# Kernel tuning notes

Measured on AMD Instinct MI355X. Metric: run time of the kernel, lower is better.

The kernel has to match this reference:

```python
import jax, jax.numpy as jnp
import numpy as np

BERT_DIM = 1024
HIDDEN = 64          # GlobalPointer head size d
NUM_TYPE = 9
MASK_NEG = 1.0e12


def _rope_sin_cos(seq_len, dim, dtype=jnp.float32):
    # sinusoidal_position_embedding: emb[s, 2i]=sin(s*w_i), emb[s,2i+1]=cos(s*w_i)
    pos = jnp.arange(seq_len, dtype=dtype)[:, None]                  # [S,1]
    inv = jnp.power(10000.0, -2.0 * jnp.arange(dim // 2, dtype=dtype) / dim)
    ang = pos * inv                                                   # [S,D/2]
    sin_pos = jnp.repeat(jnp.sin(ang), 2, axis=-1)                    # [S,D] = emb[..., ::2] interleave-2
    cos_pos = jnp.repeat(jnp.cos(ang), 2, axis=-1)                    # [S,D] = emb[..., 1::2] interleave-2
    return sin_pos, cos_pos


def _rotate(x):
    # stack([-x[...,1::2], x[...,::2]], -1).reshape(x.shape)
    x2 = jnp.stack([-x[..., 1::2], x[..., ::2]], axis=-1)
    return x2.reshape(x.shape)


def setup_inputs() -> dict:
    key = jax.random.key(0)
    k1, k2, k3 = jax.random.split(key, 3)
    B, S = 16, 512
    hidden = jax.random.normal(k1, (B, S, BERT_DIM), dtype=jnp.float32)
    attention_mask = jnp.ones((B, S), dtype=jnp.float32)
    W = jax.random.normal(k2, (BERT_DIM, NUM_TYPE * HIDDEN * 2), dtype=jnp.float32) * (1.0 / np.sqrt(BERT_DIM))
    b = jax.random.normal(k3, (NUM_TYPE * HIDDEN * 2,), dtype=jnp.float32) * 0.02
    return {"bert_last_hidden_state": hidden, "attention_mask": attention_mask, "W": W, "b": b}


def reference(bert_last_hidden_state, attention_mask, W, b):
    h = bert_last_hidden_state                                        # [B,S,bert_dim]
    B, S, _ = h.shape
    out = h @ W + b                                                   # [B,S,T*2d]
    # split into T chunks of 2d and stack on dim -2 == reshape
    out = out.reshape(B, S, NUM_TYPE, 2 * HIDDEN)
    qw, kw = out[..., :HIDDEN], out[..., HIDDEN:]                     # [B,S,T,d]
    sin_pos, cos_pos = _rope_sin_cos(S, HIDDEN, h.dtype)              # [S,d]
    sin_pos = sin_pos[None, :, None, :]                               # [1,S,1,d]
    cos_pos = cos_pos[None, :, None, :]
    qw = qw * cos_pos + _rotate(qw) * sin_pos
    kw = kw * cos_pos + _rotate(kw) * sin_pos
    logits = jnp.einsum('bmhd,bnhd->bhmn', qw, kw)                    # [B,T,S,S]
    pad = attention_mask[:, None, None, :]                            # [B,1,1,S] -> broadcast [B,T,S,S]
    logits = logits * pad - (1.0 - pad) * MASK_NEG
    return logits / jnp.sqrt(jnp.asarray(HIDDEN, logits.dtype))
```

## Files before the change

kernel.cpp:

```cpp
#include <hip/hip_runtime.h>
#include <hip/hip_bf16.h>

#define BDIM 1024
#define NCOL 1152
#define HEADS 9
#define HID 64
#define SLEN 512
#define BATCH 16

typedef __attribute__((ext_vector_type(8))) short bf16x8;
typedef __attribute__((ext_vector_type(8))) unsigned short u16x8;
typedef __attribute__((ext_vector_type(4))) float f32x4;
typedef __attribute__((ext_vector_type(4))) unsigned short u16x4;

static __device__ __forceinline__ unsigned short f2bf(float f) {
    union { float f; unsigned int u; } x; x.f = f;
    unsigned int u = x.u;
    unsigned int r = (u + 0x7fffu + ((u >> 16) & 1u)) >> 16;
    return (unsigned short)r;
}

#define GLOAD_LDS16(g, l)                                                     \
    __builtin_amdgcn_global_load_lds(                                         \
        (const __attribute__((address_space(1))) unsigned int*)(g),           \
        (__attribute__((address_space(3))) unsigned int*)(l), 16, 0, 0)

__global__ __launch_bounds__(256) void prep_kernel(const float* __restrict__ hidden,
                                                   const float* __restrict__ W,
                                                   unsigned short* __restrict__ Ab,
                                                   unsigned short* __restrict__ Wt,
                                                   float* __restrict__ sctab) {
    __shared__ float tile[32][33];
    const int b = blockIdx.x;
    if (b < 4096) {
        int i = (b * 256 + threadIdx.x) * 8;
        float4 a = *reinterpret_cast<const float4*>(hidden + i);
        float4 c = *reinterpret_cast<const float4*>(hidden + i + 4);
        u16x8 p;
        p[0] = f2bf(a.x); p[1] = f2bf(a.y); p[2] = f2bf(a.z); p[3] = f2bf(a.w);
        p[4] = f2bf(c.x); p[5] = f2bf(c.y); p[6] = f2bf(c.z); p[7] = f2bf(c.w);
        *reinterpret_cast<u16x8*>(Ab + i) = p;
    } else if (b < 5248) {
        const int bb = b - 4096;
        const int tx = threadIdx.x & 31;
        const int ty = threadIdx.x >> 5;
        const int nb = (bb % 36) * 32;
        const int kb = (bb / 36) * 32;
#pragma unroll
        for (int i = 0; i < 4; ++i) {
            int k = kb + ty + i * 8;
            tile[ty + i * 8][tx] = W[(size_t)k * NCOL + nb + tx];
        }
        __syncthreads();
#pragma unroll
        for (int i = 0; i < 4; ++i) {
            int n = nb + ty + i * 8;
            Wt[(size_t)n * BDIM + kb + tx] = f2bf(tile[tx][ty + i * 8]);
        }
    } else {
        int idx = (b - 5248) * 256 + threadIdx.x;
        int s = idx >> 5, j = idx & 31;
        float inv = powf(10000.0f, -(float)(2 * j) / (float)HID);
        float ang = (float)s * inv;
        sctab[idx * 2]     = sinf(ang);
        sctab[idx * 2 + 1] = cosf(ang);
    }
}

__global__ __launch_bounds__(512) void proj_rope_kernel(
    const unsigned short* __restrict__ Ab,
    const unsigned short* __restrict__ Wt,
    const float* __restrict__ bias,
    const float4* __restrict__ sctab4,
    unsigned short* __restrict__ qk)
{
    __shared__ __attribute__((aligned(16))) unsigned short As[2][256 * 64];
    __shared__ __attribute__((aligned(16))) unsigned short Bs[2][192 * 64];

    const int t = threadIdx.x;
    const int m0 = blockIdx.x * 256;
    const int n0 = blockIdx.y * 144;
    const int wid = t >> 6, lane = t & 63;
    const int lrow = lane & 15;
    const int lk = lane >> 4;

    const int rowoff = lane >> 3;
    const int sslot = (lane & 7) ^ rowoff;
    const unsigned short* gA = Ab + (size_t)(m0 + wid * 32 + rowoff) * BDIM + sslot * 8;
    const unsigned short* gB = Wt + (size_t)(n0 + wid * 24 + rowoff) * BDIM + sslot * 8;
    const int lA = wid * 2048;
    const int lB = wid * 1536;

#define STAGE(buf, k0)                                                        \
    do {                                                                      \
        GLOAD_LDS16(gA + (k0),             &As[buf][lA]);                     \
        GLOAD_LDS16(gA + (k0) + 8 * BDIM,  &As[buf][lA + 512]);               \
        GLOAD_LDS16(gA + (k0) + 16 * BDIM, &As[buf][lA + 1024]);              \
        GLOAD_LDS16(gA + (k0) + 24 * BDIM, &As[buf][lA + 1536]);              \
        GLOAD_LDS16(gB + (k0),             &Bs[buf][lB]);                     \
        GLOAD_LDS16(gB + (k0) + 8 * BDIM,  &Bs[buf][lB + 512]);               \
        GLOAD_LDS16(gB + (k0) + 16 * BDIM, &Bs[buf][lB + 1024]);              \
    } while (0)

    const int rkey = lrow & 7;

    f32x4 acc[9][2] = {};

    STAGE(0, 0);
    asm volatile("s_waitcnt vmcnt(0)" ::: "memory");
    __builtin_amdgcn_s_barrier();
    __builtin_amdgcn_sched_barrier(0);

    int cur = 0;
    for (int it = 0; it < 16; ++it) {
        if (it < 15) STAGE(cur ^ 1, (it + 1) * 64);
        __builtin_amdgcn_sched_barrier(0);

        const char* Ac = (const char*)As[cur];
        const char* Bc = (const char*)Bs[cur];
#pragma unroll
        for (int kk = 0; kk < 2; ++kk) {
            const int fslot = ((kk * 4 + lk) ^ rkey) << 4;
            bf16x8 af[2], bfr[9];
#pragma unroll
            for (int mi = 0; mi < 2; ++mi)
                af[mi] = *reinterpret_cast<const bf16x8*>(
                    Ac + (wid * 32 + mi * 16 + lrow) * 128 + fslot);
#pragma unroll
            for (int ni = 0; ni < 9; ++ni)
                bfr[ni] = *reinterpret_cast<const bf16x8*>(
                    Bc + (ni * 16 + lrow) * 128 + fslot);
#pragma unroll
            for (int ni = 0; ni < 9; ++ni)
#pragma unroll
                for (int mi = 0; mi < 2; ++mi)
                    acc[ni][mi] = __builtin_amdgcn_mfma_f32_16x16x32_bf16(
                        bfr[ni], af[mi], acc[ni][mi], 0, 0, 0);
        }

        if (it < 15) {
            asm volatile("s_waitcnt vmcnt(0)" ::: "memory");
            __builtin_amdgcn_s_barrier();
            __builtin_amdgcn_sched_barrier(0);
        }
        cur ^= 1;
    }
#undef STAGE

    const float4* bias4 = (const float4*)bias;
#pragma unroll
    for (int ni = 0; ni < 9; ++ni) {
        int cb = n0 + ni * 16 + lk * 4;
        float4 bv = bias4[cb >> 2];
        int h = cb >> 7;
        int qki = (cb >> 6) & 1;
        int d0 = cb & 63;
#pragma unroll
        for (int mi = 0; mi < 2; ++mi) {
            int m = m0 + wid * 32 + mi * 16 + lrow;
            int bi = m >> 9, s = m & 511;
            float4 sc = sctab4[s * 16 + (d0 >> 2)];
            f32x4 a = acc[ni][mi];
            float v0 = a[0] + bv.x, v1 = a[1] + bv.y;
            float v2 = a[2] + bv.z, v3 = a[3] + bv.w;
            u16x4 p;
            p[0] = f2bf(v0 * sc.y - v1 * sc.x);
            p[1] = f2bf(v1 * sc.y + v0 * sc.x);
            p[2] = f2bf(v2 * sc.w - v3 * sc.z);
            p[3] = f2bf(v3 * sc.w + v2 * sc.z);
            *reinterpret_cast<u16x4*>(
                qk + ((((size_t)bi * HEADS + h) * 2 + qki) * SLEN + s) * HID + d0) = p;
        }
    }
}

__global__ __launch_bounds__(256) void logits_kernel(
    const unsigned short* __restrict__ qkbuf,
    const float* __restrict__ mask,
    float* __restrict__ out)
{
    __shared__ __attribute__((aligned(16))) unsigned short Qs[128 * 72];
    __shared__ __attribute__((aligned(16))) unsigned short Ks[128 * 72];

    const int t = threadIdx.x;
    const int bz = blockIdx.z;
    const int bi = bz / 9;
    const int m0 = blockIdx.x * 128, n0 = blockIdx.y * 128;

    const unsigned short* Qg = qkbuf + ((size_t)bz * 2 + 0) * SLEN * HID + (size_t)m0 * HID;
    const unsigned short* Kg = qkbuf + ((size_t)bz * 2 + 1) * SLEN * HID + (size_t)n0 * HID;

#pragma unroll
    for (int i = 0; i < 4; ++i) {
        int e = t + i * 256;
        int row = e >> 3, c = e & 7;
        *reinterpret_cast<uint4*>(&Qs[row * 72 + c * 8]) =
            *reinterpret_cast<const uint4*>(Qg + (size_t)row * HID + c * 8);
        *reinterpret_cast<uint4*>(&Ks[row * 72 + c * 8]) =
            *reinterpret_cast<const uint4*>(Kg + (size_t)row * HID + c * 8);
    }
    __syncthreads();

    const int wid = t >> 6, lane = t & 63;
    const int wr = wid >> 1, wc = wid & 1;
    const int lrow = lane & 15;
    const int lk = lane >> 4;

    f32x4 acc[4][4] = {};
#pragma unroll
    for (int kk = 0; kk < 2; ++kk) {
        bf16x8 af[4], bfr[4];
#pragma unroll
        for (int mi = 0; mi < 4; ++mi)
            af[mi] = *reinterpret_cast<const bf16x8*>(
                &Qs[(wr * 64 + mi * 16 + lrow) * 72 + kk * 32 + lk * 8]);
#pragma unroll
        for (int ni = 0; ni < 4; ++ni)
            bfr[ni] = *reinterpret_cast<const bf16x8*>(
                &Ks[(wc * 64 + ni * 16 + lrow) * 72 + kk * 32 + lk * 8]);
#pragma unroll
        for (int ni = 0; ni < 4; ++ni)
#pragma unroll
            for (int mi = 0; mi < 4; ++mi)
                acc[ni][mi] = __builtin_amdgcn_mfma_f32_16x16x32_bf16(
                    bfr[ni], af[mi], acc[ni][mi], 0, 0, 0);
    }

#pragma unroll
    for (int ni = 0; ni < 4; ++ni) {
        int nb = n0 + wc * 64 + ni * 16 + lk * 4;
        float4 pv = *reinterpret_cast<const float4*>(mask + bi * SLEN + nb);
        float sx = (1.0f - pv.x) * 1000000000000.0f;
        float sy = (1.0f - pv.y) * 1000000000000.0f;
        float sz = (1.0f - pv.z) * 1000000000000.0f;
        float sw = (1.0f - pv.w) * 1000000000000.0f;
#pragma unroll
        for (int mi = 0; mi < 4; ++mi) {
            int m = m0 + wr * 64 + mi * 16 + lrow;
            f32x4 a = acc[ni][mi];
            f32x4 o;
            o[0] = (a[0] * pv.x - sx) * 0.125f;
            o[1] = (a[1] * pv.y - sy) * 0.125f;
            o[2] = (a[2] * pv.z - sz) * 0.125f;
            o[3] = (a[3] * pv.w - sw) * 0.125f;
            *reinterpret_cast<f32x4*>(out + ((size_t)bz * SLEN + m) * SLEN + nb) = o;
        }
    }
}

extern "C" void kernel_launch(void* const* d_in, const int* in_sizes, int n_in,
                              void* d_out, int out_size, void* d_ws, size_t ws_size,
                              hipStream_t stream) {
    const float* hidden = (const float*)d_in[0];
    const float* mask   = (const float*)d_in[1];
    const float* W      = (const float*)d_in[2];
    const float* bias   = (const float*)d_in[3];
    float* out = (float*)d_out;

    char* ws = (char*)d_ws;
    unsigned short* Ab = (unsigned short*)ws;
    unsigned short* Wt = (unsigned short*)(ws + 16777216);
    float* sctab = (float*)(ws + 16777216 + 2457600);
    unsigned short* qk = (unsigned short*)(ws + 16777216 + 2457600 + 131072);

    prep_kernel<<<5312, 256, 0, stream>>>(hidden, W, Ab, Wt, sctab);
    proj_rope_kernel<<<dim3(32, 8), 512, 0, stream>>>(
        Ab, Wt, bias, (const float4*)sctab, qk);
    logits_kernel<<<dim3(4, 4, BATCH * HEADS), 256, 0, stream>>>(qk, mask, out);
}
```

Before: 84.95 us.

## Triple-buffer projection GEMM LDS with split-phase prefetch and MFMA priority

Changes the projection GEMM from double to triple-buffered LDS staging. Prefetch runs two k-tiles ahead, with the A and B loads split across the two k sub-phases and per-wave vmcnt waits. Only the first 6 waves load B, and the B buffer shrinks to the 144 rows actually used. It also raises wave priority around the MFMA bursts and shrinks the workspace layout for Wt. The aim is to hide global-load latency behind compute, at the cost of more LDS (less occupancy headroom) and tricky wait-count correctness.

```diff
diff --git a/kernel.cpp b/kernel.cpp
--- a/kernel.cpp
+++ b/kernel.cpp
@@ -74,8 +74,8 @@
     const float4* __restrict__ sctab4,
     unsigned short* __restrict__ qk)
 {
-    __shared__ __attribute__((aligned(16))) unsigned short As[2][256 * 64];
-    __shared__ __attribute__((aligned(16))) unsigned short Bs[2][192 * 64];
+    __shared__ __attribute__((aligned(16))) unsigned short As[3][256 * 64];
+    __shared__ __attribute__((aligned(16))) unsigned short Bs[3][144 * 64];
 
     const int t = threadIdx.x;
     const int m0 = blockIdx.x * 256;
@@ -90,13 +90,17 @@
     const unsigned short* gB = Wt + (size_t)(n0 + wid * 24 + rowoff) * BDIM + sslot * 8;
     const int lA = wid * 2048;
     const int lB = wid * 1536;
-
-#define STAGE(buf, k0)                                                        \
+    const bool hasB = (wid < 6);
+
+#define STAGE_A(buf, k0)                                                      \
     do {                                                                      \
         GLOAD_LDS16(gA + (k0),             &As[buf][lA]);                     \
         GLOAD_LDS16(gA + (k0) + 8 * BDIM,  &As[buf][lA + 512]);               \
         GLOAD_LDS16(gA + (k0) + 16 * BDIM, &As[buf][lA + 1024]);              \
         GLOAD_LDS16(gA + (k0) + 24 * BDIM, &As[buf][lA + 1536]);              \
+    } while (0)
+#define STAGE_B(buf, k0)                                                      \
+    do {                                                                      \
         GLOAD_LDS16(gB + (k0),             &Bs[buf][lB]);                     \
         GLOAD_LDS16(gB + (k0) + 8 * BDIM,  &Bs[buf][lB + 512]);               \
         GLOAD_LDS16(gB + (k0) + 16 * BDIM, &Bs[buf][lB + 1024]);              \
@@ -106,21 +110,26 @@
 
     f32x4 acc[9][2] = {};
 
-    STAGE(0, 0);
-    asm volatile("s_waitcnt vmcnt(0)" ::: "memory");
-    __builtin_amdgcn_s_barrier();
-    __builtin_amdgcn_sched_barrier(0);
+    STAGE_A(0, 0);  if (hasB) STAGE_B(0, 0);
+    STAGE_A(1, 64); if (hasB) STAGE_B(1, 64);
 
     int cur = 0;
     for (int it = 0; it < 16; ++it) {
-        if (it < 15) STAGE(cur ^ 1, (it + 1) * 64);
+        if (it < 15) {
+            if (hasB) asm volatile("s_waitcnt vmcnt(7)" ::: "memory");
+            else      asm volatile("s_waitcnt vmcnt(4)" ::: "memory");
+        } else {
+            asm volatile("s_waitcnt vmcnt(0)" ::: "memory");
+        }
+        __builtin_amdgcn_s_barrier();
         __builtin_amdgcn_sched_barrier(0);
 
         const char* Ac = (const char*)As[cur];
         const char* Bc = (const char*)Bs[cur];
-#pragma unroll
-        for (int kk = 0; kk < 2; ++kk) {
-            const int fslot = ((kk * 4 + lk) ^ rkey) << 4;
+        const int nb2 = (cur + 2 >= 3) ? cur - 1 : cur + 2;
+
+        {
+            const int fslot = (lk ^ rkey) << 4;
             bf16x8 af[2], bfr[9];
 #pragma unroll
             for (int mi = 0; mi < 2; ++mi)
@@ -130,22 +139,51 @@
             for (int ni = 0; ni < 9; ++ni)
                 bfr[ni] = *reinterpret_cast<const bf16x8*>(
                     Bc + (ni * 16 + lrow) * 128 + fslot);
+            if (it < 14) STAGE_A(nb2, (it + 2) * 64);
+            __builtin_amdgcn_sched_barrier(0);
+            asm volatile("s_waitcnt lgkmcnt(0)" ::: "memory");
+            __builtin_amdgcn_sched_barrier(0);
+            __builtin_amdgcn_s_setprio(1);
 #pragma unroll
             for (int ni = 0; ni < 9; ++ni)
 #pragma unroll
                 for (int mi = 0; mi < 2; ++mi)
                     acc[ni][mi] = __builtin_amdgcn_mfma_f32_16x16x32_bf16(
                         bfr[ni], af[mi], acc[ni][mi], 0, 0, 0);
-        }
-
-        if (it < 15) {
-            asm volatile("s_waitcnt vmcnt(0)" ::: "memory");
-            __builtin_amdgcn_s_barrier();
+            __builtin_amdgcn_s_setprio(0);
+        }
+        __builtin_amdgcn_s_barrier();
+        __builtin_amdgcn_sched_barrier(0);
+
+        {
+            const int fslot = ((4 + lk) ^ rkey) << 4;
+            bf16x8 af[2], bfr[9];
+#pragma unroll
+            for (int mi = 0; mi < 2; ++mi)
+                af[mi] = *reinterpret_cast<const bf16x8*>(
+                    Ac + (wid * 32 + mi * 16 + lrow) * 128 + fslot);
+#pragma unroll
+            for (int ni = 0; ni < 9; ++ni)
+                bfr[ni] = *reinterpret_cast<const bf16x8*>(
+                    Bc + (ni * 16 + lrow) * 128 + fslot);
+            if (it < 14 && hasB) STAGE_B(nb2, (it + 2) * 64);
             __builtin_amdgcn_sched_barrier(0);
-        }
-        cur ^= 1;
-    }
-#undef STAGE
+            asm volatile("s_waitcnt lgkmcnt(0)" ::: "memory");
+            __builtin_amdgcn_sched_barrier(0);
+            __builtin_amdgcn_s_setprio(1);
+#pragma unroll
+            for (int ni = 0; ni < 9; ++ni)
+#pragma unroll
+                for (int mi = 0; mi < 2; ++mi)
+                    acc[ni][mi] = __builtin_amdgcn_mfma_f32_16x16x32_bf16(
+                        bfr[ni], af[mi], acc[ni][mi], 0, 0, 0);
+            __builtin_amdgcn_s_setprio(0);
+        }
+
+        cur = (cur + 1 >= 3) ? 0 : cur + 1;
+    }
+#undef STAGE_A
+#undef STAGE_B
 
     const float4* bias4 = (const float4*)bias;
 #pragma unroll
@@ -260,8 +298,8 @@
     char* ws = (char*)d_ws;
     unsigned short* Ab = (unsigned short*)ws;
     unsigned short* Wt = (unsigned short*)(ws + 16777216);
-    float* sctab = (float*)(ws + 16777216 + 2457600);
-    unsigned short* qk = (unsigned short*)(ws + 16777216 + 2457600 + 131072);
+    float* sctab = (float*)(ws + 16777216 + 2359296);
+    unsigned short* qk = (unsigned short*)(ws + 16777216 + 2359296 + 131072);
 
     prep_kernel<<<5312, 256, 0, stream>>>(hidden, W, Ab, Wt, sctab);
     proj_rope_kernel<<<dim3(32, 8), 512, 0, stream>>>(
```

After: 79.05 us. 7.0% less time.

## Shrink projection GEMM tiles to 128 rows and drop LDS double buffering

Applied to the files above, without the earlier changes.

The projection GEMM moves from 256x144 tiles with 512 threads and double-buffered LDS to 128x144 tiles with 256 threads and a single LDS buffer. Each K step now loads and then synchronizes with __syncthreads, and B rows are split unevenly across the four waves (5/5/4/4 row groups). The aim is to double the block count (512 blocks instead of 256) to fill more of the CUs, and to allow several blocks per CU through smaller LDS use and the launch bound. The cost is that global loads no longer overlap with MFMA work inside a block, and each K step needs two barriers. Workspace offsets are also shifted down.

```diff
diff --git a/kernel.cpp b/kernel.cpp
--- a/kernel.cpp
+++ b/kernel.cpp
@@ -67,18 +67,18 @@
     }
 }
 
-__global__ __launch_bounds__(512) void proj_rope_kernel(
+__global__ __launch_bounds__(256, 3) void proj_rope_kernel(
     const unsigned short* __restrict__ Ab,
     const unsigned short* __restrict__ Wt,
     const float* __restrict__ bias,
     const float4* __restrict__ sctab4,
     unsigned short* __restrict__ qk)
 {
-    __shared__ __attribute__((aligned(16))) unsigned short As[2][256 * 64];
-    __shared__ __attribute__((aligned(16))) unsigned short Bs[2][192 * 64];
+    __shared__ __attribute__((aligned(16))) unsigned short As[128 * 64];
+    __shared__ __attribute__((aligned(16))) unsigned short Bs[144 * 64];
 
     const int t = threadIdx.x;
-    const int m0 = blockIdx.x * 256;
+    const int m0 = blockIdx.x * 128;
     const int n0 = blockIdx.y * 144;
     const int wid = t >> 6, lane = t & 63;
     const int lrow = lane & 15;
@@ -87,37 +87,29 @@
     const int rowoff = lane >> 3;
     const int sslot = (lane & 7) ^ rowoff;
     const unsigned short* gA = Ab + (size_t)(m0 + wid * 32 + rowoff) * BDIM + sslot * 8;
-    const unsigned short* gB = Wt + (size_t)(n0 + wid * 24 + rowoff) * BDIM + sslot * 8;
+    const int bbase = (wid < 2) ? wid * 40 : 80 + (wid - 2) * 32;
+    const int bcnt  = (wid < 2) ? 5 : 4;
+    const unsigned short* gB = Wt + (size_t)(n0 + bbase + rowoff) * BDIM + sslot * 8;
     const int lA = wid * 2048;
-    const int lB = wid * 1536;
-
-#define STAGE(buf, k0)                                                        \
-    do {                                                                      \
-        GLOAD_LDS16(gA + (k0),             &As[buf][lA]);                     \
-        GLOAD_LDS16(gA + (k0) + 8 * BDIM,  &As[buf][lA + 512]);               \
-        GLOAD_LDS16(gA + (k0) + 16 * BDIM, &As[buf][lA + 1024]);              \
-        GLOAD_LDS16(gA + (k0) + 24 * BDIM, &As[buf][lA + 1536]);              \
-        GLOAD_LDS16(gB + (k0),             &Bs[buf][lB]);                     \
-        GLOAD_LDS16(gB + (k0) + 8 * BDIM,  &Bs[buf][lB + 512]);               \
-        GLOAD_LDS16(gB + (k0) + 16 * BDIM, &Bs[buf][lB + 1024]);              \
-    } while (0)
+    const int lB = bbase * 64;
 
     const int rkey = lrow & 7;
 
     f32x4 acc[9][2] = {};
 
-    STAGE(0, 0);
-    asm volatile("s_waitcnt vmcnt(0)" ::: "memory");
-    __builtin_amdgcn_s_barrier();
-    __builtin_amdgcn_sched_barrier(0);
-
-    int cur = 0;
     for (int it = 0; it < 16; ++it) {
-        if (it < 15) STAGE(cur ^ 1, (it + 1) * 64);
-        __builtin_amdgcn_sched_barrier(0);
-
-        const char* Ac = (const char*)As[cur];
-        const char* Bc = (const char*)Bs[cur];
+        const int k0 = it * 64;
+#pragma unroll
+        for (int i = 0; i < 4; ++i)
+            GLOAD_LDS16(gA + k0 + i * 8 * BDIM, &As[lA + i * 512]);
+#pragma unroll
+        for (int i = 0; i < 5; ++i)
+            if (i < bcnt)
+                GLOAD_LDS16(gB + k0 + i * 8 * BDIM, &Bs[lB + i * 512]);
+        __syncthreads();
+
+        const char* Ac = (const char*)As;
+        const char* Bc = (const char*)Bs;
 #pragma unroll
         for (int kk = 0; kk < 2; ++kk) {
             const int fslot = ((kk * 4 + lk) ^ rkey) << 4;
@@ -137,15 +129,8 @@
                     acc[ni][mi] = __builtin_amdgcn_mfma_f32_16x16x32_bf16(
                         bfr[ni], af[mi], acc[ni][mi], 0, 0, 0);
         }
-
-        if (it < 15) {
-            asm volatile("s_waitcnt vmcnt(0)" ::: "memory");
-            __builtin_amdgcn_s_barrier();
-            __builtin_amdgcn_sched_barrier(0);
-        }
-        cur ^= 1;
-    }
-#undef STAGE
+        __syncthreads();
+    }
 
     const float4* bias4 = (const float4*)bias;
 #pragma unroll
@@ -260,11 +245,11 @@
     char* ws = (char*)d_ws;
     unsigned short* Ab = (unsigned short*)ws;
     unsigned short* Wt = (unsigned short*)(ws + 16777216);
-    float* sctab = (float*)(ws + 16777216 + 2457600);
-    unsigned short* qk = (unsigned short*)(ws + 16777216 + 2457600 + 131072);
+    float* sctab = (float*)(ws + 16777216 + 2359296);
+    unsigned short* qk = (unsigned short*)(ws + 16777216 + 2359296 + 131072);
 
     prep_kernel<<<5312, 256, 0, stream>>>(hidden, W, Ab, Wt, sctab);
-    proj_rope_kernel<<<dim3(32, 8), 512, 0, stream>>>(
+    proj_rope_kernel<<<dim3(64, 8), 256, 0, stream>>>(
         Ab, Wt, bias, (const float4*)sctab, qk);
     logits_kernel<<<dim3(4, 4, BATCH * HEADS), 256, 0, stream>>>(qk, mask, out);
 }
```

Result: faster. 80.91 us (-4.8%).
